# Kernel optimization log

Measured on AMD Instinct MI355X. Metric: run time of the kernel, lower is better.

Reference implementation:

```python
import jax, jax.numpy as jnp
import numpy as np

T, D, FF, E, R = 4096, 1024, 2048, 4, 16
LORA_SCALE = 32.0 / 16.0  # alpha / r


def setup_inputs() -> dict:
    key = jax.random.key(0)
    ks = jax.random.split(key, 12)
    return {
        "x": jax.random.normal(ks[0], (T, D), jnp.float32),
        "gate_w": jax.random.normal(ks[1], (E, D), jnp.float32) * 0.03,
        "gate_up_w": jax.random.normal(ks[2], (D, 2 * FF), jnp.float32)[None].repeat(E, 0) * 0.0
                     + jax.random.normal(ks[2], (E, D, 2 * FF), jnp.float32) * 0.03,
        "gate_up_b": jax.random.normal(ks[3], (E, 2 * FF), jnp.float32) * 0.01,
        "down_w": jax.random.normal(ks[4], (E, FF, D), jnp.float32) * 0.02,
        "down_b": jax.random.normal(ks[5], (E, D), jnp.float32) * 0.01,
        "A_gate": jax.random.normal(ks[6], (E, R, D), jnp.float32) * 0.02,
        "B_gate": jax.random.normal(ks[7], (E, FF, R), jnp.float32) * 0.02,
        "A_up": jax.random.normal(ks[8], (E, R, D), jnp.float32) * 0.02,
        "B_up": jax.random.normal(ks[9], (E, FF, R), jnp.float32) * 0.02,
        "A_down": jax.random.normal(ks[10], (E, R, FF), jnp.float32) * 0.02,
        "B_down": jax.random.normal(ks[11], (E, D, R), jnp.float32) * 0.02,
        "top_k": 2,
    }


def reference(x, gate_w, gate_up_w, gate_up_b, down_w, down_b,
              A_gate, B_gate, A_up, B_up, A_down, B_down, top_k):
    t, d = x.shape
    e = gate_w.shape[0]
    # --- router: logits, softmax (fp32), top-k, renormalize ---
    router_logits = x @ gate_w.T                                   # [T,E]
    rw = jax.nn.softmax(router_logits.astype(jnp.float32), axis=1)
    top_w, sel = jax.lax.top_k(rw, top_k)                          # [T,k]
    top_w = top_w / jnp.sum(top_w, axis=-1, keepdims=True)
    top_w = top_w.astype(x.dtype)
    # dense per-token per-expert combine weights (scatter of top-k weights)
    w = jnp.zeros((t, e), x.dtype).at[jnp.arange(t)[:, None], sel].add(top_w)  # [T,E]
    # --- per-expert SwiGLU MLP with LoRA (vectorized over experts) ---
    gu = jnp.einsum('td,edf->etf', x, gate_up_w) + gate_up_b[:, None, :]       # [E,T,2FF]
    ff = gu.shape[-1] // 2
    gate = gu[..., :ff] + jnp.einsum('td,erd,efr->etf', x, A_gate, B_gate) * LORA_SCALE
    up = gu[..., ff:] + jnp.einsum('td,erd,efr->etf', x, A_up, B_up) * LORA_SCALE
    act = jax.nn.silu(gate) * up                                               # [E,T,FF]
    down = jnp.einsum('etf,efd->etd', act, down_w) + down_b[:, None, :]
    down = down + jnp.einsum('etf,erf,edr->etd', act, A_down, B_down) * LORA_SCALE
    # --- weighted scatter-combine ---
    final = jnp.einsum('etd,te->td', down, w)                                  # [T,D]
    return final, router_logits
```

## Files before the change

kernel.cpp:

```cpp
#include <hip/hip_runtime.h>

#define T_TOK 4096
#define DIM   1024
#define FFD   2048
#define NEXP  4
#define NRP   9216

typedef unsigned short u16;
typedef __attribute__((ext_vector_type(8))) short short8;
typedef __attribute__((ext_vector_type(4))) float f32x4;
typedef __attribute__((ext_vector_type(8))) unsigned short u16x8;
typedef __attribute__((ext_vector_type(4))) unsigned short u16x4;

typedef __attribute__((address_space(1))) unsigned int as1_u32;
typedef __attribute__((address_space(3))) unsigned int as3_u32;

__device__ __forceinline__ u16 f2bf(float f) {
  union { float f; unsigned u; } v; v.f = f;
  unsigned u = v.u;
  return (u16)((u + 0x7fffu + ((u >> 16) & 1u)) >> 16);
}
__device__ __forceinline__ float bf2f(u16 h) {
  union { unsigned u; float f; } v; v.u = ((unsigned)h) << 16;
  return v.f;
}
__device__ __forceinline__ void gload16(const void* g, void* l) {
  __builtin_amdgcn_global_load_lds((const as1_u32*)g, (as3_u32*)l, 16, 0, 0);
}

__global__ void router_k(const float* __restrict__ x, const float* __restrict__ gw,
                         float* __restrict__ logits_out, int* __restrict__ sel,
                         float* __restrict__ selw) {
  int t = blockIdx.x;
  int lane = threadIdx.x;
  float xv[16];
#pragma unroll
  for (int i = 0; i < 16; ++i) xv[i] = x[(size_t)t * DIM + lane + i * 64];
  float l[4];
#pragma unroll
  for (int e = 0; e < 4; ++e) {
    float s = 0.f;
#pragma unroll
    for (int i = 0; i < 16; ++i) s += xv[i] * gw[e * DIM + lane + i * 64];
#pragma unroll
    for (int off = 32; off > 0; off >>= 1) s += __shfl_xor(s, off, 64);
    l[e] = s;
  }
  if (lane == 0) {
#pragma unroll
    for (int e = 0; e < 4; ++e) logits_out[(size_t)t * 4 + e] = l[e];
    int e0 = 0; float b0 = l[0];
    for (int e = 1; e < 4; ++e) if (l[e] > b0) { b0 = l[e]; e0 = e; }
    int e1 = -1; float b1 = -3.4e38f;
    for (int e = 0; e < 4; ++e) if (e != e0 && l[e] > b1) { b1 = l[e]; e1 = e; }
    float p1 = expf(b1 - b0);
    float w0 = 1.f / (1.f + p1);
    sel[2 * t] = e0; sel[2 * t + 1] = e1;
    selw[2 * t] = w0; selw[2 * t + 1] = 1.f - w0;
  }
}

__global__ void scan_k(const int* __restrict__ sel, int* __restrict__ pos,
                       int* __restrict__ offs, int* __restrict__ rowtok,
                       int* __restrict__ pairrow) {
  __shared__ int base[4];
  __shared__ int wsum[16][4];
  __shared__ int off_s[5];
  int tid = threadIdx.x, lane = tid & 63, wid = tid >> 6;
  if (tid < 4) base[tid] = 0;
  __syncthreads();
  for (int chunk = 0; chunk < 4; ++chunk) {
    int t = chunk * 1024 + tid;
    int e0 = sel[2 * t], e1 = sel[2 * t + 1];
    unsigned long long ltm = (1ull << lane) - 1ull;
    bool f[4]; int within[4];
#pragma unroll
    for (int e = 0; e < 4; ++e) {
      f[e] = (e0 == e) || (e1 == e);
      unsigned long long m = __ballot(f[e]);
      within[e] = __popcll(m & ltm);
      if (lane == 0) wsum[wid][e] = __popcll(m);
    }
    __syncthreads();
    int wbase[4] = {0, 0, 0, 0}, tot[4] = {0, 0, 0, 0};
    for (int i = 0; i < 16; ++i)
#pragma unroll
      for (int e = 0; e < 4; ++e) {
        int v = wsum[i][e];
        if (i < wid) wbase[e] += v;
        tot[e] += v;
      }
#pragma unroll
    for (int e = 0; e < 4; ++e)
      if (f[e]) {
        int p = base[e] + wbase[e] + within[e];
        if (e0 == e) pos[2 * t] = p; else pos[2 * t + 1] = p;
      }
    __syncthreads();
    if (tid < 4) base[tid] += tot[tid];
    __syncthreads();
  }
  if (tid == 0) {
    int o = 0;
    for (int e = 0; e < 4; ++e) { off_s[e] = o; o += ((base[e] + 255) >> 8) << 8; }
    off_s[4] = o;
    for (int i = 0; i < 5; ++i) offs[i] = off_s[i];
  }
  __syncthreads();
  for (int r = tid; r < NRP; r += 1024) rowtok[r] = -1;
  __syncthreads();
  for (int t = tid; t < T_TOK; t += 1024) {
#pragma unroll
    for (int s = 0; s < 2; ++s) {
      int e = sel[2 * t + s];
      int rr = off_s[e] + pos[2 * t + s];
      pairrow[2 * t + s] = rr;
      rowtok[rr] = t;
    }
  }
}

__global__ void gather_k(const float* __restrict__ x, const int* __restrict__ rowtok,
                         u16* __restrict__ xg) {
  int r = blockIdx.x, tid = threadIdx.x;
  int t = rowtok[r];
  float4 v = make_float4(0.f, 0.f, 0.f, 0.f);
  if (t >= 0) v = ((const float4*)(x + (size_t)t * DIM))[tid];
  u16x4 o;
  o[0] = f2bf(v.x); o[1] = f2bf(v.y); o[2] = f2bf(v.z); o[3] = f2bf(v.w);
  ((u16x4*)(xg + (size_t)r * DIM))[tid] = o;
}

__global__ void cvtA_k(const float* __restrict__ Ag, const float* __restrict__ Au,
                       const float* __restrict__ Ad, u16* __restrict__ abgu,
                       u16* __restrict__ adb) {
  int g = blockIdx.x * 256 + threadIdx.x;
  if (g < 32768) {
    int flat = g * 4;
    int e = flat >> 15;
    int rem = flat & 32767;
    int q = rem >> 10;
    int d = rem & 1023;
    const float* src = (q < 16) ? (Ag + ((size_t)e * 16 + q) * DIM + d)
                                : (Au + ((size_t)e * 16 + (q - 16)) * DIM + d);
    float4 v = *(const float4*)src;
    u16x4 o; o[0] = f2bf(v.x); o[1] = f2bf(v.y); o[2] = f2bf(v.z); o[3] = f2bf(v.w);
    *(u16x4*)(abgu + (size_t)flat) = o;
  } else {
    int flat = (g - 32768) * 4;
    float4 v = *(const float4*)(Ad + flat);
    u16x4 o; o[0] = f2bf(v.x); o[1] = f2bf(v.y); o[2] = f2bf(v.z); o[3] = f2bf(v.w);
    *(u16x4*)(adb + (size_t)flat) = o;
  }
}

__global__ void xa_k(const u16* __restrict__ xg, const u16* __restrict__ abgu,
                     const int* __restrict__ offs, float* __restrict__ xagu) {
  int r0 = blockIdx.x * 2, lane = threadIdx.x;
  int e = 0;
  if (r0 >= offs[1]) e = 1;
  if (r0 >= offs[2]) e = 2;
  if (r0 >= offs[3]) e = 3;
  float x0[16], x1[16];
#pragma unroll
  for (int i = 0; i < 4; ++i) {
    u16x4 v0 = ((const u16x4*)(xg + (size_t)r0 * DIM))[lane + i * 64];
    u16x4 v1 = ((const u16x4*)(xg + (size_t)(r0 + 1) * DIM))[lane + i * 64];
#pragma unroll
    for (int j = 0; j < 4; ++j) { x0[i * 4 + j] = bf2f(v0[j]); x1[i * 4 + j] = bf2f(v1[j]); }
  }
  const u16* A = abgu + (size_t)e * 32 * DIM;
  for (int q = 0; q < 32; ++q) {
    float s0 = 0.f, s1 = 0.f;
#pragma unroll
    for (int i = 0; i < 4; ++i) {
      u16x4 av = ((const u16x4*)(A + (size_t)q * DIM))[lane + i * 64];
#pragma unroll
      for (int j = 0; j < 4; ++j) {
        float a = bf2f(av[j]);
        s0 += x0[i * 4 + j] * a; s1 += x1[i * 4 + j] * a;
      }
    }
#pragma unroll
    for (int off = 32; off > 0; off >>= 1) { s0 += __shfl_xor(s0, off, 64); s1 += __shfl_xor(s1, off, 64); }
    if (lane == 0) { xagu[(size_t)r0 * 32 + q] = s0; xagu[(size_t)(r0 + 1) * 32 + q] = s1; }
  }
}

__global__ void aad_k(const u16* __restrict__ act, const u16* __restrict__ adb,
                      const int* __restrict__ offs, float* __restrict__ aad) {
  int r0 = blockIdx.x * 2, lane = threadIdx.x;
  int e = 0;
  if (r0 >= offs[1]) e = 1;
  if (r0 >= offs[2]) e = 2;
  if (r0 >= offs[3]) e = 3;
  float x0[32], x1[32];
#pragma unroll
  for (int i = 0; i < 8; ++i) {
    u16x4 v0 = ((const u16x4*)(act + (size_t)r0 * FFD))[lane + i * 64];
    u16x4 v1 = ((const u16x4*)(act + (size_t)(r0 + 1) * FFD))[lane + i * 64];
#pragma unroll
    for (int j = 0; j < 4; ++j) { x0[i * 4 + j] = bf2f(v0[j]); x1[i * 4 + j] = bf2f(v1[j]); }
  }
  const u16* A = adb + (size_t)e * 16 * FFD;
  for (int q = 0; q < 16; ++q) {
    float s0 = 0.f, s1 = 0.f;
#pragma unroll
    for (int i = 0; i < 8; ++i) {
      u16x4 av = ((const u16x4*)(A + (size_t)q * FFD))[lane + i * 64];
#pragma unroll
      for (int j = 0; j < 4; ++j) {
        float a = bf2f(av[j]);
        s0 += x0[i * 4 + j] * a; s1 += x1[i * 4 + j] * a;
      }
    }
#pragma unroll
    for (int off = 32; off > 0; off >>= 1) { s0 += __shfl_xor(s0, off, 64); s1 += __shfl_xor(s1, off, 64); }
    if (lane == 0) { aad[(size_t)r0 * 16 + q] = s0; aad[(size_t)(r0 + 1) * 16 + q] = s1; }
  }
}

__global__ void transpose_k(const float* __restrict__ in, u16* __restrict__ out,
                            int K, int N) {
  int e = blockIdx.z;
  int n0 = blockIdx.x * 32, k0 = blockIdx.y * 32;
  const float* I = in + (size_t)e * K * N;
  u16* O = out + (size_t)e * N * K;
  __shared__ u16 tile[32][33];
#pragma unroll
  for (int i = 0; i < 4; ++i) {
    int k = k0 + threadIdx.y + i * 8;
    tile[threadIdx.y + i * 8][threadIdx.x] = f2bf(I[(size_t)k * N + n0 + threadIdx.x]);
  }
  __syncthreads();
#pragma unroll
  for (int i = 0; i < 4; ++i) {
    int n = n0 + threadIdx.y + i * 8;
    O[(size_t)n * K + k0 + threadIdx.x] = tile[threadIdx.x][threadIdx.y + i * 8];
  }
}

__global__ __launch_bounds__(512, 2) void gemm1_k(
    const u16* __restrict__ xg, const u16* __restrict__ wgu_t,
    const float* __restrict__ gub, const float* __restrict__ Bg,
    const float* __restrict__ Bu, const float* __restrict__ xagu,
    const int* __restrict__ offs, u16* __restrict__ act) {
  __shared__ __align__(16) u16 sAB[65536];
  int tid = threadIdx.x, w = tid >> 6, lane = tid & 63;
  int f0 = blockIdx.x * 128;
  int row0 = blockIdx.y * 256;
  int e = 0;
  if (row0 >= offs[1]) e = 1;
  if (row0 >= offs[2]) e = 2;
  if (row0 >= offs[3]) e = 3;
  int wm = w >> 2, wn = w & 3;

  int srow = w * 16 + (lane >> 2);
  int scol = ((lane & 3) ^ ((lane >> 3) & 3)) * 8;
  const u16* gA0 = xg + (size_t)(row0 + srow) * DIM + scol;
  const u16* gA1 = gA0 + (size_t)128 * DIM;
  const u16* gBg = wgu_t + ((size_t)e << 22) + (size_t)(f0 + srow) * DIM + scol;
  const u16* gBu = wgu_t + ((size_t)e << 22) + (size_t)(2048 + f0 + srow) * DIM + scol;

  int fo = ((lane >> 4) ^ ((lane >> 1) & 3)) * 8;
  int ard = (wm * 128 + (lane & 15)) * 32 + fo;
  int brd = 8192 + (wn * 64 + (lane & 15)) * 32 + fo;

  f32x4 acc[8][4];
#pragma unroll
  for (int i = 0; i < 8; ++i)
#pragma unroll
    for (int j = 0; j < 4; ++j) acc[i][j] = f32x4{0.f, 0.f, 0.f, 0.f};

#pragma unroll
  for (int p = 0; p < 2; ++p) {
    u16* s = sAB + p * 16384 + w * 512;
    gload16(gA0 + p * 32, s);
    gload16(gA1 + p * 32, s + 4096);
    gload16(gBg + p * 32, s + 8192);
    gload16(gBu + p * 32, s + 12288);
  }

#pragma unroll
  for (int k = 0; k < 32; ++k) {
    const u16* cb = sAB + (k & 3) * 16384;
    if (k == 31) asm volatile("s_waitcnt vmcnt(0)" ::: "memory");
    else         asm volatile("s_waitcnt vmcnt(4)" ::: "memory");
    __builtin_amdgcn_s_barrier();
    short8 a[4], b[4];
#pragma unroll
    for (int ni = 0; ni < 4; ++ni) b[ni] = *(const short8*)&cb[brd + ni * 512];
#pragma unroll
    for (int fr = 0; fr < 4; ++fr) a[fr] = *(const short8*)&cb[ard + fr * 512];
    if (k + 2 < 32) {
      u16* s = sAB + ((k + 2) & 3) * 16384 + w * 512;
      gload16(gA0 + (k + 2) * 32, s);
      gload16(gA1 + (k + 2) * 32, s + 4096);
    }
    asm volatile("s_waitcnt lgkmcnt(0)" ::: "memory");
    __builtin_amdgcn_sched_barrier(0);
    __builtin_amdgcn_s_setprio(1);
#pragma unroll
    for (int fr = 0; fr < 4; ++fr)
#pragma unroll
      for (int ni = 0; ni < 4; ++ni)
        acc[fr][ni] = __builtin_amdgcn_mfma_f32_16x16x32_bf16(a[fr], b[ni], acc[fr][ni], 0, 0, 0);
    __builtin_amdgcn_s_setprio(0);
    __builtin_amdgcn_s_barrier();
#pragma unroll
    for (int fr = 0; fr < 4; ++fr) a[fr] = *(const short8*)&cb[ard + (fr + 4) * 512];
    if (k + 2 < 32) {
      u16* s = sAB + ((k + 2) & 3) * 16384 + w * 512;
      gload16(gBg + (k + 2) * 32, s + 8192);
      gload16(gBu + (k + 2) * 32, s + 12288);
    }
    asm volatile("s_waitcnt lgkmcnt(0)" ::: "memory");
    __builtin_amdgcn_sched_barrier(0);
    __builtin_amdgcn_s_setprio(1);
#pragma unroll
    for (int fr = 0; fr < 4; ++fr)
#pragma unroll
      for (int ni = 0; ni < 4; ++ni)
        acc[fr + 4][ni] = __builtin_amdgcn_mfma_f32_16x16x32_bf16(a[fr], b[ni], acc[fr + 4][ni], 0, 0, 0);
    __builtin_amdgcn_s_setprio(0);
    __builtin_amdgcn_s_barrier();
  }

  __syncthreads();
  {
    int c = tid >> 8, r = tid & 255;
    int key = (r >> 1) & 3;
    u16* A = sAB + c * 16384 + r * 32;
    u16 tmp[16];
#pragma unroll
    for (int q = 0; q < 16; ++q) tmp[q] = f2bf(2.f * xagu[(size_t)(row0 + r) * 32 + c * 16 + q]);
    u16 one8[8] = {0x3f80, 0, 0, 0, 0, 0, 0, 0};
    u16 z8[8] = {0, 0, 0, 0, 0, 0, 0, 0};
    *(u16x8*)&A[(0 ^ key) * 8] = *(u16x8*)&tmp[0];
    *(u16x8*)&A[(1 ^ key) * 8] = *(u16x8*)&tmp[8];
    *(u16x8*)&A[(2 ^ key) * 8] = *(u16x8*)&one8[0];
    *(u16x8*)&A[(3 ^ key) * 8] = *(u16x8*)&z8[0];
    if (tid < 256) {
      int rb = tid;
      int keyb = (rb >> 1) & 3;
      u16* B = sAB + 8192 + rb * 32;
      const float* Bsrc = (rb < 128) ? Bg : Bu;
      int fb = (rb < 128) ? rb : (rb - 128);
      float bias = gub[e * 4096 + ((rb < 128) ? (f0 + fb) : (2048 + f0 + fb))];
      u16 tb[16];
#pragma unroll
      for (int q = 0; q < 16; ++q) tb[q] = f2bf(Bsrc[((size_t)e * FFD + f0 + fb) * 16 + q]);
      u16 bb8[8] = {f2bf(bias), 0, 0, 0, 0, 0, 0, 0};
      *(u16x8*)&B[(0 ^ keyb) * 8] = *(u16x8*)&tb[0];
      *(u16x8*)&B[(1 ^ keyb) * 8] = *(u16x8*)&tb[8];
      *(u16x8*)&B[(2 ^ keyb) * 8] = *(u16x8*)&bb8[0];
      *(u16x8*)&B[(3 ^ keyb) * 8] = *(u16x8*)&z8[0];
    }
  }
  __syncthreads();
  {
    const u16* ca = sAB + (wn < 2 ? 0 : 16384);
    short8 a[8], b[4];
#pragma unroll
    for (int ni = 0; ni < 4; ++ni) b[ni] = *(const short8*)&sAB[brd + ni * 512];
#pragma unroll
    for (int fr = 0; fr < 8; ++fr) a[fr] = *(const short8*)&ca[ard + fr * 512];
#pragma unroll
    for (int fr = 0; fr < 8; ++fr)
#pragma unroll
      for (int ni = 0; ni < 4; ++ni)
        acc[fr][ni] = __builtin_amdgcn_mfma_f32_16x16x32_bf16(a[fr], b[ni], acc[fr][ni], 0, 0, 0);
  }
  __syncthreads();
#pragma unroll
  for (int fr = 0; fr < 8; ++fr)
#pragma unroll
    for (int ni = 0; ni < 4; ++ni)
#pragma unroll
      for (int j = 0; j < 4; ++j) {
        int row = wm * 128 + fr * 16 + (lane >> 4) * 4 + j;
        int col = wn * 64 + ni * 16 + (lane & 15);
        int key = ((row & 3) ^ ((row >> 2) & 3)) << 4;
        sAB[row * 256 + (col ^ key)] = f2bf(acc[fr][ni][j]);
      }
  __syncthreads();
  {
    int fc = (tid & 15) * 8;
    int rb = tid >> 4;
#pragma unroll
    for (int it = 0; it < 8; ++it) {
      int row = rb + it * 32;
      int key = ((row & 3) ^ ((row >> 2) & 3)) << 4;
      u16x8 gv = *(const u16x8*)&sAB[row * 256 + (fc ^ key)];
      u16x8 uv = *(const u16x8*)&sAB[row * 256 + ((fc + 128) ^ key)];
      u16x8 ov;
#pragma unroll
      for (int j = 0; j < 8; ++j) {
        float g = bf2f(gv[j]);
        float u = bf2f(uv[j]);
        float s = g / (1.f + __expf(-g));
        ov[j] = f2bf(s * u);
      }
      *(u16x8*)(act + (size_t)(row0 + row) * FFD + f0 + fc) = ov;
    }
  }
}

__global__ __launch_bounds__(512, 2) void gemm2_k(
    const u16* __restrict__ act, const u16* __restrict__ wd_t,
    const float* __restrict__ db, const float* __restrict__ Bd,
    const float* __restrict__ aad, const int* __restrict__ offs,
    u16* __restrict__ down) {
  __shared__ __align__(16) u16 sAB[65536];
  int tid = threadIdx.x, w = tid >> 6, lane = tid & 63;
  int n0 = blockIdx.x * 256;
  int row0 = blockIdx.y * 256;
  int ks = blockIdx.z;
  size_t kbase = (size_t)ks * 1024;
  int e = 0;
  if (row0 >= offs[1]) e = 1;
  if (row0 >= offs[2]) e = 2;
  if (row0 >= offs[3]) e = 3;
  int wm = w >> 2, wn = w & 3;

  int srow = w * 16 + (lane >> 2);
  int scol = ((lane & 3) ^ ((lane >> 3) & 3)) * 8;
  const u16* gA0 = act + (size_t)(row0 + srow) * FFD + kbase + scol;
  const u16* gA1 = gA0 + (size_t)128 * FFD;
  const u16* gB0 = wd_t + (size_t)e * DIM * FFD + (size_t)(n0 + srow) * FFD + kbase + scol;
  const u16* gB1 = gB0 + (size_t)128 * FFD;

  int fo = ((lane >> 4) ^ ((lane >> 1) & 3)) * 8;
  int ard = (wm * 128 + (lane & 15)) * 32 + fo;
  int brd = 8192 + (wn * 64 + (lane & 15)) * 32 + fo;

  f32x4 acc[8][4];
#pragma unroll
  for (int i = 0; i < 8; ++i)
#pragma unroll
    for (int j = 0; j < 4; ++j) acc[i][j] = f32x4{0.f, 0.f, 0.f, 0.f};

#pragma unroll
  for (int p = 0; p < 2; ++p) {
    u16* s = sAB + p * 16384 + w * 512;
    gload16(gA0 + p * 32, s);
    gload16(gA1 + p * 32, s + 4096);
    gload16(gB0 + p * 32, s + 8192);
    gload16(gB1 + p * 32, s + 12288);
  }

#pragma unroll
  for (int k = 0; k < 32; ++k) {
    const u16* cb = sAB + (k & 3) * 16384;
    if (k == 31) asm volatile("s_waitcnt vmcnt(0)" ::: "memory");
    else         asm volatile("s_waitcnt vmcnt(4)" ::: "memory");
    __builtin_amdgcn_s_barrier();
    short8 a[4], b[4];
#pragma unroll
    for (int ni = 0; ni < 4; ++ni) b[ni] = *(const short8*)&cb[brd + ni * 512];
#pragma unroll
    for (int fr = 0; fr < 4; ++fr) a[fr] = *(const short8*)&cb[ard + fr * 512];
    if (k + 2 < 32) {
      u16* s = sAB + ((k + 2) & 3) * 16384 + w * 512;
      gload16(gA0 + (k + 2) * 32, s);
      gload16(gA1 + (k + 2) * 32, s + 4096);
    }
    asm volatile("s_waitcnt lgkmcnt(0)" ::: "memory");
    __builtin_amdgcn_sched_barrier(0);
    __builtin_amdgcn_s_setprio(1);
#pragma unroll
    for (int fr = 0; fr < 4; ++fr)
#pragma unroll
      for (int ni = 0; ni < 4; ++ni)
        acc[fr][ni] = __builtin_amdgcn_mfma_f32_16x16x32_bf16(a[fr], b[ni], acc[fr][ni], 0, 0, 0);
    __builtin_amdgcn_s_setprio(0);
    __builtin_amdgcn_s_barrier();
#pragma unroll
    for (int fr = 0; fr < 4; ++fr) a[fr] = *(const short8*)&cb[ard + (fr + 4) * 512];
    if (k + 2 < 32) {
      u16* s = sAB + ((k + 2) & 3) * 16384 + w * 512;
      gload16(gB0 + (k + 2) * 32, s + 8192);
      gload16(gB1 + (k + 2) * 32, s + 12288);
    }
    asm volatile("s_waitcnt lgkmcnt(0)" ::: "memory");
    __builtin_amdgcn_sched_barrier(0);
    __builtin_amdgcn_s_setprio(1);
#pragma unroll
    for (int fr = 0; fr < 4; ++fr)
#pragma unroll
      for (int ni = 0; ni < 4; ++ni)
        acc[fr + 4][ni] = __builtin_amdgcn_mfma_f32_16x16x32_bf16(a[fr], b[ni], acc[fr + 4][ni], 0, 0, 0);
    __builtin_amdgcn_s_setprio(0);
    __builtin_amdgcn_s_barrier();
  }

  if (ks == 0) {
    __syncthreads();
    if (tid < 256) {
      int r = tid;
      int key = (r >> 1) & 3;
      u16* A = sAB + r * 32;
      u16 tmp[16];
#pragma unroll
      for (int q = 0; q < 16; ++q) tmp[q] = f2bf(2.f * aad[(size_t)(row0 + r) * 16 + q]);
      u16 one8[8] = {0x3f80, 0, 0, 0, 0, 0, 0, 0};
      u16 z8[8] = {0, 0, 0, 0, 0, 0, 0, 0};
      *(u16x8*)&A[(0 ^ key) * 8] = *(u16x8*)&tmp[0];
      *(u16x8*)&A[(1 ^ key) * 8] = *(u16x8*)&tmp[8];
      *(u16x8*)&A[(2 ^ key) * 8] = *(u16x8*)&one8[0];
      *(u16x8*)&A[(3 ^ key) * 8] = *(u16x8*)&z8[0];
      u16* B = sAB + 8192 + r * 32;
      u16 tb[16];
#pragma unroll
      for (int q = 0; q < 16; ++q) tb[q] = f2bf(Bd[((size_t)e * DIM + n0 + r) * 16 + q]);
      u16 bb8[8] = {f2bf(db[e * DIM + n0 + r]), 0, 0, 0, 0, 0, 0, 0};
      *(u16x8*)&B[(0 ^ key) * 8] = *(u16x8*)&tb[0];
      *(u16x8*)&B[(1 ^ key) * 8] = *(u16x8*)&tb[8];
      *(u16x8*)&B[(2 ^ key) * 8] = *(u16x8*)&bb8[0];
      *(u16x8*)&B[(3 ^ key) * 8] = *(u16x8*)&z8[0];
    }
    __syncthreads();
    {
      short8 a[8], b[4];
#pragma unroll
      for (int ni = 0; ni < 4; ++ni) b[ni] = *(const short8*)&sAB[brd + ni * 512];
#pragma unroll
      for (int fr = 0; fr < 8; ++fr) a[fr] = *(const short8*)&sAB[ard + fr * 512];
#pragma unroll
      for (int fr = 0; fr < 8; ++fr)
#pragma unroll
        for (int ni = 0; ni < 4; ++ni)
          acc[fr][ni] = __builtin_amdgcn_mfma_f32_16x16x32_bf16(a[fr], b[ni], acc[fr][ni], 0, 0, 0);
    }
  }
#pragma unroll
  for (int fr = 0; fr < 8; ++fr)
#pragma unroll
    for (int ni = 0; ni < 4; ++ni)
#pragma unroll
      for (int j = 0; j < 4; ++j) {
        int lr = wm * 128 + fr * 16 + (lane >> 4) * 4 + j;
        int lc = wn * 64 + ni * 16 + (lane & 15);
        down[((size_t)ks * NRP + row0 + lr) * DIM + n0 + lc] = f2bf(acc[fr][ni][j]);
      }
}

__global__ void combine_k(const u16* __restrict__ down, const int* __restrict__ pairrow,
                          const float* __restrict__ selw, float* __restrict__ out) {
  int t = blockIdx.x, tid = threadIdx.x;
  int r0 = pairrow[2 * t], r1 = pairrow[2 * t + 1];
  float w0 = selw[2 * t], w1 = selw[2 * t + 1];
  u16x4 a0 = *(const u16x4*)(down + ((size_t)r0) * DIM + tid * 4);
  u16x4 a1 = *(const u16x4*)(down + ((size_t)NRP + r0) * DIM + tid * 4);
  u16x4 b0 = *(const u16x4*)(down + ((size_t)r1) * DIM + tid * 4);
  u16x4 b1 = *(const u16x4*)(down + ((size_t)NRP + r1) * DIM + tid * 4);
  f32x4 o;
#pragma unroll
  for (int j = 0; j < 4; ++j)
    o[j] = w0 * (bf2f(a0[j]) + bf2f(a1[j])) + w1 * (bf2f(b0[j]) + bf2f(b1[j]));
  *(f32x4*)(out + (size_t)t * DIM + tid * 4) = o;
}

extern "C" void kernel_launch(void* const* d_in, const int* in_sizes, int n_in,
                              void* d_out, int out_size, void* d_ws, size_t ws_size,
                              hipStream_t stream) {
  const float* x         = (const float*)d_in[0];
  const float* gate_w    = (const float*)d_in[1];
  const float* gate_up_w = (const float*)d_in[2];
  const float* gate_up_b = (const float*)d_in[3];
  const float* down_w    = (const float*)d_in[4];
  const float* down_b    = (const float*)d_in[5];
  const float* A_gate    = (const float*)d_in[6];
  const float* B_gate    = (const float*)d_in[7];
  const float* A_up      = (const float*)d_in[8];
  const float* B_up      = (const float*)d_in[9];
  const float* A_down    = (const float*)d_in[10];
  const float* B_down    = (const float*)d_in[11];

  float* out_final  = (float*)d_out;
  float* out_logits = out_final + (size_t)T_TOK * DIM;

  char* ws = (char*)d_ws;
  size_t o = 0;
  auto take = [&](size_t bytes) -> void* {
    void* p = ws + o;
    o = (o + bytes + 255) & ~(size_t)255;
    return p;
  };
  int*   offs    = (int*)take(64);
  int*   sel     = (int*)take((size_t)T_TOK * 2 * 4);
  float* selw    = (float*)take((size_t)T_TOK * 2 * 4);
  int*   pos     = (int*)take((size_t)T_TOK * 2 * 4);
  int*   pairrow = (int*)take((size_t)T_TOK * 2 * 4);
  int*   rowtok  = (int*)take((size_t)NRP * 4);
  float* xagu    = (float*)take((size_t)NRP * 32 * 4);
  float* aadb    = (float*)take((size_t)NRP * 16 * 4);
  u16*   abgu    = (u16*)take((size_t)NEXP * 32 * DIM * 2);
  u16*   adb     = (u16*)take((size_t)NEXP * 16 * FFD * 2);
  u16*   xg      = (u16*)take((size_t)NRP * DIM * 2);
  u16*   actb    = (u16*)take((size_t)NRP * FFD * 2);
  u16*   downb   = (u16*)take((size_t)2 * NRP * DIM * 2);
  u16*   wgu_t   = (u16*)take((size_t)NEXP * 2 * FFD * DIM * 2);
  u16*   wd_t    = (u16*)take((size_t)NEXP * DIM * FFD * 2);
  (void)ws_size; (void)in_sizes; (void)n_in; (void)out_size;

  transpose_k<<<dim3(128, 32, NEXP), dim3(32, 8), 0, stream>>>(gate_up_w, wgu_t, DIM, 2 * FFD);
  transpose_k<<<dim3(32, 64, NEXP), dim3(32, 8), 0, stream>>>(down_w, wd_t, FFD, DIM);
  cvtA_k<<<256, 256, 0, stream>>>(A_gate, A_up, A_down, abgu, adb);

  router_k<<<T_TOK, 64, 0, stream>>>(x, gate_w, out_logits, sel, selw);
  scan_k<<<1, 1024, 0, stream>>>(sel, pos, offs, rowtok, pairrow);
  gather_k<<<NRP, 256, 0, stream>>>(x, rowtok, xg);
  xa_k<<<NRP / 2, 64, 0, stream>>>(xg, abgu, offs, xagu);
  gemm1_k<<<dim3(16, NRP / 256), 512, 0, stream>>>(xg, wgu_t, gate_up_b, B_gate, B_up,
                                                   xagu, offs, actb);
  aad_k<<<NRP / 2, 64, 0, stream>>>(actb, adb, offs, aadb);
  gemm2_k<<<dim3(4, NRP / 256, 2), 512, 0, stream>>>(actb, wd_t, down_b, B_down, aadb,
                                                     offs, downb);
  combine_k<<<T_TOK, 256, 0, stream>>>(downb, pairrow, selw, out_final);
}
```

Measured before the change: 287.4 us.

## Restructure expert GEMMs to 4-wave blocks with 128x128 warp tiles and register double-buffering

Both expert GEMM kernels move from 8 waves at 2 blocks per CU to 4 waves at 1 block per CU. Each wave now computes a 128x128 tile with 64 accumulators instead of 128x64. The K-loop is rewritten as a 3-stage LDS ring that keeps two stages of global loads in flight, and LDS-to-register fragment reads are double-buffered so the next step's reads overlap the current MFMAs. This aims to raise per-wave data reuse and cut barrier and LDS-read overhead, at the cost of much higher register pressure, lower occupancy and less latency hiding across waves.

Result: slower. 317.7 us (+10.6%).

```diff
diff --git a/kernel.cpp b/kernel.cpp
--- a/kernel.cpp
+++ b/kernel.cpp
@@ -5,6 +5,7 @@
 #define FFD   2048
 #define NEXP  4
 #define NRP   9216
+#define NTILES 36
 
 typedef unsigned short u16;
 typedef __attribute__((ext_vector_type(8))) short short8;
@@ -240,7 +241,7 @@
   }
 }
 
-__global__ __launch_bounds__(512, 2) void gemm1_k(
+__global__ __launch_bounds__(256, 1) void gemm1_k(
     const u16* __restrict__ xg, const u16* __restrict__ wgu_t,
     const float* __restrict__ gub, const float* __restrict__ Bg,
     const float* __restrict__ Bu, const float* __restrict__ xagu,
@@ -253,133 +254,126 @@
   if (row0 >= offs[1]) e = 1;
   if (row0 >= offs[2]) e = 2;
   if (row0 >= offs[3]) e = 3;
-  int wm = w >> 2, wn = w & 3;
-
-  int srow = w * 16 + (lane >> 2);
+  int wm = w >> 1, wn = w & 1;
+
+  int srow = lane >> 2;
   int scol = ((lane & 3) ^ ((lane >> 3) & 3)) * 8;
-  const u16* gA0 = xg + (size_t)(row0 + srow) * DIM + scol;
-  const u16* gA1 = gA0 + (size_t)128 * DIM;
-  const u16* gBg = wgu_t + ((size_t)e << 22) + (size_t)(f0 + srow) * DIM + scol;
-  const u16* gBu = wgu_t + ((size_t)e << 22) + (size_t)(2048 + f0 + srow) * DIM + scol;
+  const u16* gA = xg + (size_t)(row0 + w * 16 + srow) * DIM + scol;
+  const u16* gBb = wgu_t + ((size_t)e << 22);
+  const u16* gB01 = gBb + (size_t)(f0 + w * 16 + srow) * DIM + scol;
+  const u16* gB23 = gBb + (size_t)(2048 + f0 + w * 16 + srow) * DIM + scol;
 
   int fo = ((lane >> 4) ^ ((lane >> 1) & 3)) * 8;
   int ard = (wm * 128 + (lane & 15)) * 32 + fo;
-  int brd = 8192 + (wn * 64 + (lane & 15)) * 32 + fo;
-
-  f32x4 acc[8][4];
+  int brd = 8192 + (wn * 128 + (lane & 15)) * 32 + fo;
+
+  f32x4 acc[8][8];
 #pragma unroll
   for (int i = 0; i < 8; ++i)
 #pragma unroll
-    for (int j = 0; j < 4; ++j) acc[i][j] = f32x4{0.f, 0.f, 0.f, 0.f};
-
-#pragma unroll
-  for (int p = 0; p < 2; ++p) {
-    u16* s = sAB + p * 16384 + w * 512;
-    gload16(gA0 + p * 32, s);
-    gload16(gA1 + p * 32, s + 4096);
-    gload16(gBg + p * 32, s + 8192);
-    gload16(gBu + p * 32, s + 12288);
-  }
-
-#pragma unroll
-  for (int k = 0; k < 32; ++k) {
-    const u16* cb = sAB + (k & 3) * 16384;
-    if (k == 31) asm volatile("s_waitcnt vmcnt(0)" ::: "memory");
-    else         asm volatile("s_waitcnt vmcnt(4)" ::: "memory");
-    __builtin_amdgcn_s_barrier();
-    short8 a[4], b[4];
-#pragma unroll
-    for (int ni = 0; ni < 4; ++ni) b[ni] = *(const short8*)&cb[brd + ni * 512];
-#pragma unroll
-    for (int fr = 0; fr < 4; ++fr) a[fr] = *(const short8*)&cb[ard + fr * 512];
-    if (k + 2 < 32) {
-      u16* s = sAB + ((k + 2) & 3) * 16384 + w * 512;
-      gload16(gA0 + (k + 2) * 32, s);
-      gload16(gA1 + (k + 2) * 32, s + 4096);
-    }
-    asm volatile("s_waitcnt lgkmcnt(0)" ::: "memory");
-    __builtin_amdgcn_sched_barrier(0);
-    __builtin_amdgcn_s_setprio(1);
-#pragma unroll
-    for (int fr = 0; fr < 4; ++fr)
-#pragma unroll
-      for (int ni = 0; ni < 4; ++ni)
-        acc[fr][ni] = __builtin_amdgcn_mfma_f32_16x16x32_bf16(a[fr], b[ni], acc[fr][ni], 0, 0, 0);
-    __builtin_amdgcn_s_setprio(0);
-    __builtin_amdgcn_s_barrier();
-#pragma unroll
-    for (int fr = 0; fr < 4; ++fr) a[fr] = *(const short8*)&cb[ard + (fr + 4) * 512];
-    if (k + 2 < 32) {
-      u16* s = sAB + ((k + 2) & 3) * 16384 + w * 512;
-      gload16(gBg + (k + 2) * 32, s + 8192);
-      gload16(gBu + (k + 2) * 32, s + 12288);
-    }
-    asm volatile("s_waitcnt lgkmcnt(0)" ::: "memory");
-    __builtin_amdgcn_sched_barrier(0);
-    __builtin_amdgcn_s_setprio(1);
-#pragma unroll
-    for (int fr = 0; fr < 4; ++fr)
-#pragma unroll
-      for (int ni = 0; ni < 4; ++ni)
-        acc[fr + 4][ni] = __builtin_amdgcn_mfma_f32_16x16x32_bf16(a[fr], b[ni], acc[fr + 4][ni], 0, 0, 0);
-    __builtin_amdgcn_s_setprio(0);
-    __builtin_amdgcn_s_barrier();
+    for (int j = 0; j < 8; ++j) acc[i][j] = f32x4{0.f, 0.f, 0.f, 0.f};
+
+  auto STAGE = [&](int k) {
+    u16* dA = sAB + (k % 3) * 16384 + w * 512;
+    const u16* a = gA + k * 32;
+    gload16(a, dA);
+    gload16(a + 64 * DIM, dA + 2048);
+    gload16(a + 128 * DIM, dA + 4096);
+    gload16(a + 192 * DIM, dA + 6144);
+    u16* dB = sAB + (k % 3) * 16384 + 8192 + w * 512;
+    const u16* b0 = gB01 + k * 32;
+    const u16* b2 = gB23 + k * 32;
+    gload16(b0, dB);
+    gload16(b0 + 64 * DIM, dB + 2048);
+    gload16(b2, dB + 4096);
+    gload16(b2 + 64 * DIM, dB + 6144);
+  };
+  auto READS = [&](int k, short8* a8, short8* b8) {
+    const u16* cb = sAB + (k % 3) * 16384;
+#pragma unroll
+    for (int fr = 0; fr < 8; ++fr) a8[fr] = *(const short8*)&cb[ard + fr * 512];
+#pragma unroll
+    for (int ni = 0; ni < 8; ++ni) b8[ni] = *(const short8*)&cb[brd + ni * 512];
+  };
+  auto MM = [&](short8* a8, short8* b8) {
+#pragma unroll
+    for (int fr = 0; fr < 8; ++fr)
+#pragma unroll
+      for (int ni = 0; ni < 8; ++ni)
+        acc[fr][ni] = __builtin_amdgcn_mfma_f32_16x16x32_bf16(a8[fr], b8[ni], acc[fr][ni], 0, 0, 0);
+  };
+
+  short8 af0[8], bf0[8], af1[8], bf1[8];
+  STAGE(0); STAGE(1);
+  asm volatile("s_waitcnt vmcnt(8)" ::: "memory");
+  __builtin_amdgcn_s_barrier();
+  READS(0, af0, bf0);
+#pragma unroll
+  for (int t = 0; t < 32; ++t) {
+    if (t < 30) STAGE(t + 2);
+    if (t < 31) {
+      if (t == 30) asm volatile("s_waitcnt vmcnt(0)" ::: "memory");
+      else         asm volatile("s_waitcnt vmcnt(8)" ::: "memory");
+      __builtin_amdgcn_s_barrier();
+    }
+    if (t & 1) {
+      if (t < 31) READS(t + 1, af0, bf0);
+      MM(af1, bf1);
+    } else {
+      if (t < 31) READS(t + 1, af1, bf1);
+      MM(af0, bf0);
+    }
   }
 
   __syncthreads();
   {
-    int c = tid >> 8, r = tid & 255;
+    int r = tid;
     int key = (r >> 1) & 3;
-    u16* A = sAB + c * 16384 + r * 32;
-    u16 tmp[16];
-#pragma unroll
-    for (int q = 0; q < 16; ++q) tmp[q] = f2bf(2.f * xagu[(size_t)(row0 + r) * 32 + c * 16 + q]);
     u16 one8[8] = {0x3f80, 0, 0, 0, 0, 0, 0, 0};
     u16 z8[8] = {0, 0, 0, 0, 0, 0, 0, 0};
-    *(u16x8*)&A[(0 ^ key) * 8] = *(u16x8*)&tmp[0];
-    *(u16x8*)&A[(1 ^ key) * 8] = *(u16x8*)&tmp[8];
-    *(u16x8*)&A[(2 ^ key) * 8] = *(u16x8*)&one8[0];
-    *(u16x8*)&A[(3 ^ key) * 8] = *(u16x8*)&z8[0];
-    if (tid < 256) {
-      int rb = tid;
-      int keyb = (rb >> 1) & 3;
-      u16* B = sAB + 8192 + rb * 32;
-      const float* Bsrc = (rb < 128) ? Bg : Bu;
-      int fb = (rb < 128) ? rb : (rb - 128);
-      float bias = gub[e * 4096 + ((rb < 128) ? (f0 + fb) : (2048 + f0 + fb))];
-      u16 tb[16];
-#pragma unroll
-      for (int q = 0; q < 16; ++q) tb[q] = f2bf(Bsrc[((size_t)e * FFD + f0 + fb) * 16 + q]);
-      u16 bb8[8] = {f2bf(bias), 0, 0, 0, 0, 0, 0, 0};
-      *(u16x8*)&B[(0 ^ keyb) * 8] = *(u16x8*)&tb[0];
-      *(u16x8*)&B[(1 ^ keyb) * 8] = *(u16x8*)&tb[8];
-      *(u16x8*)&B[(2 ^ keyb) * 8] = *(u16x8*)&bb8[0];
-      *(u16x8*)&B[(3 ^ keyb) * 8] = *(u16x8*)&z8[0];
-    }
+#pragma unroll
+    for (int h = 0; h < 2; ++h) {
+      u16* A = sAB + h * 16384 + r * 32;
+      u16 tmp[16];
+#pragma unroll
+      for (int q = 0; q < 16; ++q) tmp[q] = f2bf(2.f * xagu[(size_t)(row0 + r) * 32 + h * 16 + q]);
+      *(u16x8*)&A[(0 ^ key) * 8] = *(u16x8*)&tmp[0];
+      *(u16x8*)&A[(1 ^ key) * 8] = *(u16x8*)&tmp[8];
+      *(u16x8*)&A[(2 ^ key) * 8] = *(u16x8*)&one8[0];
+      *(u16x8*)&A[(3 ^ key) * 8] = *(u16x8*)&z8[0];
+    }
+    u16* B = sAB + 8192 + r * 32;
+    const float* Bsrc = (r < 128) ? Bg : Bu;
+    int fb = r & 127;
+    float bias = gub[e * 4096 + ((r < 128) ? (f0 + fb) : (2048 + f0 + fb))];
+    u16 tb[16];
+#pragma unroll
+    for (int q = 0; q < 16; ++q) tb[q] = f2bf(Bsrc[((size_t)e * FFD + f0 + fb) * 16 + q]);
+    u16 bb8[8] = {f2bf(bias), 0, 0, 0, 0, 0, 0, 0};
+    *(u16x8*)&B[(0 ^ key) * 8] = *(u16x8*)&tb[0];
+    *(u16x8*)&B[(1 ^ key) * 8] = *(u16x8*)&tb[8];
+    *(u16x8*)&B[(2 ^ key) * 8] = *(u16x8*)&bb8[0];
+    *(u16x8*)&B[(3 ^ key) * 8] = *(u16x8*)&z8[0];
   }
   __syncthreads();
   {
-    const u16* ca = sAB + (wn < 2 ? 0 : 16384);
-    short8 a[8], b[4];
-#pragma unroll
-    for (int ni = 0; ni < 4; ++ni) b[ni] = *(const short8*)&sAB[brd + ni * 512];
-#pragma unroll
-    for (int fr = 0; fr < 8; ++fr) a[fr] = *(const short8*)&ca[ard + fr * 512];
-#pragma unroll
-    for (int fr = 0; fr < 8; ++fr)
-#pragma unroll
-      for (int ni = 0; ni < 4; ++ni)
-        acc[fr][ni] = __builtin_amdgcn_mfma_f32_16x16x32_bf16(a[fr], b[ni], acc[fr][ni], 0, 0, 0);
+    const u16* ca = sAB + (wn ? 16384 : 0);
+    short8 a8[8], b8[8];
+#pragma unroll
+    for (int fr = 0; fr < 8; ++fr) a8[fr] = *(const short8*)&ca[ard + fr * 512];
+#pragma unroll
+    for (int ni = 0; ni < 8; ++ni) b8[ni] = *(const short8*)&sAB[brd + ni * 512];
+    MM(a8, b8);
   }
   __syncthreads();
 #pragma unroll
   for (int fr = 0; fr < 8; ++fr)
 #pragma unroll
-    for (int ni = 0; ni < 4; ++ni)
+    for (int ni = 0; ni < 8; ++ni)
 #pragma unroll
       for (int j = 0; j < 4; ++j) {
         int row = wm * 128 + fr * 16 + (lane >> 4) * 4 + j;
-        int col = wn * 64 + ni * 16 + (lane & 15);
+        int col = wn * 128 + ni * 16 + (lane & 15);
         int key = ((row & 3) ^ ((row >> 2) & 3)) << 4;
         sAB[row * 256 + (col ^ key)] = f2bf(acc[fr][ni][j]);
       }
@@ -388,8 +382,8 @@
     int fc = (tid & 15) * 8;
     int rb = tid >> 4;
 #pragma unroll
-    for (int it = 0; it < 8; ++it) {
-      int row = rb + it * 32;
+    for (int it = 0; it < 16; ++it) {
+      int row = rb + it * 16;
       int key = ((row & 3) ^ ((row >> 2) & 3)) << 4;
       u16x8 gv = *(const u16x8*)&sAB[row * 256 + (fc ^ key)];
       u16x8 uv = *(const u16x8*)&sAB[row * 256 + ((fc + 128) ^ key)];
@@ -406,12 +400,12 @@
   }
 }
 
-__global__ __launch_bounds__(512, 2) void gemm2_k(
+__global__ __launch_bounds__(256, 1) void gemm2_k(
     const u16* __restrict__ act, const u16* __restrict__ wd_t,
     const float* __restrict__ db, const float* __restrict__ Bd,
     const float* __restrict__ aad, const int* __restrict__ offs,
     u16* __restrict__ down) {
-  __shared__ __align__(16) u16 sAB[65536];
+  __shared__ __align__(16) u16 sAB[49152];
   int tid = threadIdx.x, w = tid >> 6, lane = tid & 63;
   int n0 = blockIdx.x * 256;
   int row0 = blockIdx.y * 256;
@@ -421,90 +415,85 @@
   if (row0 >= offs[1]) e = 1;
   if (row0 >= offs[2]) e = 2;
   if (row0 >= offs[3]) e = 3;
-  int wm = w >> 2, wn = w & 3;
-
-  int srow = w * 16 + (lane >> 2);
+  int wm = w >> 1, wn = w & 1;
+
+  int srow = lane >> 2;
   int scol = ((lane & 3) ^ ((lane >> 3) & 3)) * 8;
-  const u16* gA0 = act + (size_t)(row0 + srow) * FFD + kbase + scol;
-  const u16* gA1 = gA0 + (size_t)128 * FFD;
-  const u16* gB0 = wd_t + (size_t)e * DIM * FFD + (size_t)(n0 + srow) * FFD + kbase + scol;
-  const u16* gB1 = gB0 + (size_t)128 * FFD;
+  const u16* gA = act + (size_t)(row0 + w * 16 + srow) * FFD + kbase + scol;
+  const u16* gB = wd_t + (size_t)e * DIM * FFD + (size_t)(n0 + w * 16 + srow) * FFD + kbase + scol;
 
   int fo = ((lane >> 4) ^ ((lane >> 1) & 3)) * 8;
   int ard = (wm * 128 + (lane & 15)) * 32 + fo;
-  int brd = 8192 + (wn * 64 + (lane & 15)) * 32 + fo;
-
-  f32x4 acc[8][4];
+  int brd = 8192 + (wn * 128 + (lane & 15)) * 32 + fo;
+
+  f32x4 acc[8][8];
 #pragma unroll
   for (int i = 0; i < 8; ++i)
 #pragma unroll
-    for (int j = 0; j < 4; ++j) acc[i][j] = f32x4{0.f, 0.f, 0.f, 0.f};
-
-#pragma unroll
-  for (int p = 0; p < 2; ++p) {
-    u16* s = sAB + p * 16384 + w * 512;
-    gload16(gA0 + p * 32, s);
-    gload16(gA1 + p * 32, s + 4096);
-    gload16(gB0 + p * 32, s + 8192);
-    gload16(gB1 + p * 32, s + 12288);
-  }
-
-#pragma unroll
-  for (int k = 0; k < 32; ++k) {
-    const u16* cb = sAB + (k & 3) * 16384;
-    if (k == 31) asm volatile("s_waitcnt vmcnt(0)" ::: "memory");
-    else         asm volatile("s_waitcnt vmcnt(4)" ::: "memory");
-    __builtin_amdgcn_s_barrier();
-    short8 a[4], b[4];
-#pragma unroll
-    for (int ni = 0; ni < 4; ++ni) b[ni] = *(const short8*)&cb[brd + ni * 512];
-#pragma unroll
-    for (int fr = 0; fr < 4; ++fr) a[fr] = *(const short8*)&cb[ard + fr * 512];
-    if (k + 2 < 32) {
-      u16* s = sAB + ((k + 2) & 3) * 16384 + w * 512;
-      gload16(gA0 + (k + 2) * 32, s);
-      gload16(gA1 + (k + 2) * 32, s + 4096);
-    }
-    asm volatile("s_waitcnt lgkmcnt(0)" ::: "memory");
-    __builtin_amdgcn_sched_barrier(0);
-    __builtin_amdgcn_s_setprio(1);
-#pragma unroll
-    for (int fr = 0; fr < 4; ++fr)
-#pragma unroll
-      for (int ni = 0; ni < 4; ++ni)
-        acc[fr][ni] = __builtin_amdgcn_mfma_f32_16x16x32_bf16(a[fr], b[ni], acc[fr][ni], 0, 0, 0);
-    __builtin_amdgcn_s_setprio(0);
-    __builtin_amdgcn_s_barrier();
-#pragma unroll
-    for (int fr = 0; fr < 4; ++fr) a[fr] = *(const short8*)&cb[ard + (fr + 4) * 512];
-    if (k + 2 < 32) {
-      u16* s = sAB + ((k + 2) & 3) * 16384 + w * 512;
-      gload16(gB0 + (k + 2) * 32, s + 8192);
-      gload16(gB1 + (k + 2) * 32, s + 12288);
-    }
-    asm volatile("s_waitcnt lgkmcnt(0)" ::: "memory");
-    __builtin_amdgcn_sched_barrier(0);
-    __builtin_amdgcn_s_setprio(1);
-#pragma unroll
-    for (int fr = 0; fr < 4; ++fr)
-#pragma unroll
-      for (int ni = 0; ni < 4; ++ni)
-        acc[fr + 4][ni] = __builtin_amdgcn_mfma_f32_16x16x32_bf16(a[fr], b[ni], acc[fr + 4][ni], 0, 0, 0);
-    __builtin_amdgcn_s_setprio(0);
-    __builtin_amdgcn_s_barrier();
+    for (int j = 0; j < 8; ++j) acc[i][j] = f32x4{0.f, 0.f, 0.f, 0.f};
+
+  auto STAGE = [&](int k) {
+    u16* dA = sAB + (k % 3) * 16384 + w * 512;
+    const u16* a = gA + k * 32;
+    gload16(a, dA);
+    gload16(a + 64 * FFD, dA + 2048);
+    gload16(a + 128 * FFD, dA + 4096);
+    gload16(a + 192 * FFD, dA + 6144);
+    u16* dB = sAB + (k % 3) * 16384 + 8192 + w * 512;
+    const u16* b = gB + k * 32;
+    gload16(b, dB);
+    gload16(b + 64 * FFD, dB + 2048);
+    gload16(b + 128 * FFD, dB + 4096);
+    gload16(b + 192 * FFD, dB + 6144);
+  };
+  auto READS = [&](int k, short8* a8, short8* b8) {
+    const u16* cb = sAB + (k % 3) * 16384;
+#pragma unroll
+    for (int fr = 0; fr < 8; ++fr) a8[fr] = *(const short8*)&cb[ard + fr * 512];
+#pragma unroll
+    for (int ni = 0; ni < 8; ++ni) b8[ni] = *(const short8*)&cb[brd + ni * 512];
+  };
+  auto MM = [&](short8* a8, short8* b8) {
+#pragma unroll
+    for (int fr = 0; fr < 8; ++fr)
+#pragma unroll
+      for (int ni = 0; ni < 8; ++ni)
+        acc[fr][ni] = __builtin_amdgcn_mfma_f32_16x16x32_bf16(a8[fr], b8[ni], acc[fr][ni], 0, 0, 0);
+  };
+
+  short8 af0[8], bf0[8], af1[8], bf1[8];
+  STAGE(0); STAGE(1);
+  asm volatile("s_waitcnt vmcnt(8)" ::: "memory");
+  __builtin_amdgcn_s_barrier();
+  READS(0, af0, bf0);
+#pragma unroll
+  for (int t = 0; t < 32; ++t) {
+    if (t < 30) STAGE(t + 2);
+    if (t < 31) {
+      if (t == 30) asm volatile("s_waitcnt vmcnt(0)" ::: "memory");
+      else         asm volatile("s_waitcnt vmcnt(8)" ::: "memory");
+      __builtin_amdgcn_s_barrier();
+    }
+    if (t & 1) {
+      if (t < 31) READS(t + 1, af0, bf0);
+      MM(af1, bf1);
+    } else {
+      if (t < 31) READS(t + 1, af1, bf1);
+      MM(af0, bf0);
+    }
   }
 
   if (ks == 0) {
     __syncthreads();
-    if (tid < 256) {
+    {
       int r = tid;
       int key = (r >> 1) & 3;
+      u16 one8[8] = {0x3f80, 0, 0, 0, 0, 0, 0, 0};
+      u16 z8[8] = {0, 0, 0, 0, 0, 0, 0, 0};
       u16* A = sAB + r * 32;
       u16 tmp[16];
 #pragma unroll
       for (int q = 0; q < 16; ++q) tmp[q] = f2bf(2.f * aad[(size_t)(row0 + r) * 16 + q]);
-      u16 one8[8] = {0x3f80, 0, 0, 0, 0, 0, 0, 0};
-      u16 z8[8] = {0, 0, 0, 0, 0, 0, 0, 0};
       *(u16x8*)&A[(0 ^ key) * 8] = *(u16x8*)&tmp[0];
       *(u16x8*)&A[(1 ^ key) * 8] = *(u16x8*)&tmp[8];
       *(u16x8*)&A[(2 ^ key) * 8] = *(u16x8*)&one8[0];
@@ -521,26 +510,22 @@
     }
     __syncthreads();
     {
-      short8 a[8], b[4];
-#pragma unroll
-      for (int ni = 0; ni < 4; ++ni) b[ni] = *(const short8*)&sAB[brd + ni * 512];
-#pragma unroll
-      for (int fr = 0; fr < 8; ++fr) a[fr] = *(const short8*)&sAB[ard + fr * 512];
-#pragma unroll
-      for (int fr = 0; fr < 8; ++fr)
-#pragma unroll
-        for (int ni = 0; ni < 4; ++ni)
-          acc[fr][ni] = __builtin_amdgcn_mfma_f32_16x16x32_bf16(a[fr], b[ni], acc[fr][ni], 0, 0, 0);
+      short8 a8[8], b8[8];
+#pragma unroll
+      for (int fr = 0; fr < 8; ++fr) a8[fr] = *(const short8*)&sAB[ard + fr * 512];
+#pragma unroll
+      for (int ni = 0; ni < 8; ++ni) b8[ni] = *(const short8*)&sAB[brd + ni * 512];
+      MM(a8, b8);
     }
   }
 #pragma unroll
   for (int fr = 0; fr < 8; ++fr)
 #pragma unroll
-    for (int ni = 0; ni < 4; ++ni)
+    for (int ni = 0; ni < 8; ++ni)
 #pragma unroll
       for (int j = 0; j < 4; ++j) {
         int lr = wm * 128 + fr * 16 + (lane >> 4) * 4 + j;
-        int lc = wn * 64 + ni * 16 + (lane & 15);
+        int lc = wn * 128 + ni * 16 + (lane & 15);
         down[((size_t)ks * NRP + row0 + lr) * DIM + n0 + lc] = f2bf(acc[fr][ni][j]);
       }
 }
@@ -612,10 +597,10 @@
   scan_k<<<1, 1024, 0, stream>>>(sel, pos, offs, rowtok, pairrow);
   gather_k<<<NRP, 256, 0, stream>>>(x, rowtok, xg);
   xa_k<<<NRP / 2, 64, 0, stream>>>(xg, abgu, offs, xagu);
-  gemm1_k<<<dim3(16, NRP / 256), 512, 0, stream>>>(xg, wgu_t, gate_up_b, B_gate, B_up,
-                                                   xagu, offs, actb);
+  gemm1_k<<<dim3(16, NTILES), 256, 0, stream>>>(xg, wgu_t, gate_up_b, B_gate, B_up,
+                                                xagu, offs, actb);
   aad_k<<<NRP / 2, 64, 0, stream>>>(actb, adb, offs, aadb);
-  gemm2_k<<<dim3(4, NRP / 256, 2), 512, 0, stream>>>(actb, wd_t, down_b, B_down, aadb,
-                                                     offs, downb);
+  gemm2_k<<<dim3(4, NTILES, 2), 256, 0, stream>>>(actb, wd_t, down_b, B_down, aadb,
+                                                  offs, downb);
   combine_k<<<T_TOK, 256, 0, stream>>>(downb, pairrow, selw, out_final);
 }
```
